# Kernel optimization log

Hardware: AMD Instinct MI355X
Metric: run time of the kernel (lower is better)

Reference implementation:

```python
import jax, jax.numpy as jnp
import numpy as np

B, N, H = 512, 100, 768
I = 2 * H  # intermediate_dim default = hidden_dim * 2
NUM_ANS = 16
MAX_ANS = 15
LN_EPS = 1e-5


def setup_inputs() -> dict:
    key = jax.random.key(0)
    ks = jax.random.split(key, 7)
    s = 0.02
    return {
        "v_emb": jax.random.normal(ks[0], (B, N, H), dtype=jnp.float32),
        "W1": jax.random.normal(ks[1], (H, I), dtype=jnp.float32) * s,
        "b1": jax.random.normal(ks[2], (I,), dtype=jnp.float32) * s,
        "gamma": jnp.ones((I,), dtype=jnp.float32),
        "beta": jnp.zeros((I,), dtype=jnp.float32),
        "W2": jax.random.normal(ks[3], (I, 1), dtype=jnp.float32) * s,
        "b2": jax.random.normal(ks[4], (1,), dtype=jnp.float32) * s,
    }


def reference(v_emb, W1, b1, gamma, beta, W2, b2):
    # Linear -> GELU (exact/erf, torch nn.GELU default) -> LayerNorm -> Linear
    h = jnp.einsum("bnh,hi->bni", v_emb, W1) + b1            # [B,N,I]
    h = jax.nn.gelu(h, approximate=False)
    mu = jnp.mean(h, axis=-1, keepdims=True)
    var = jnp.mean(jnp.square(h - mu), axis=-1, keepdims=True)
    h = (h - mu) * jax.lax.rsqrt(var + LN_EPS) * gamma + beta
    scores = jnp.einsum("bni,io->bno", h, W2) + b2           # [B,N,1]
    scores = jax.nn.sigmoid(scores)                           # sigmoid=True branch
    pred = jnp.sum(scores, axis=1)                            # [B,1]
    # pred_to_logits: vectorized round + clamp + one-hot scatter
    # str(int(round(p))) in {'0'..'15'} -> that id; negative -> 0; overflow -> max_ans
    aid = jnp.clip(jnp.round(pred[:, 0]).astype(jnp.int32), 0, MAX_ANS)
    logits = jax.nn.one_hot(aid, NUM_ANS, dtype=scores.dtype)  # [B,16]
    # original returns dict: scores, final_attention_map (==scores), pred, logits
    return scores, pred, logits
```

## Files before the change

### kernel.cpp

```cpp
#include <hip/hip_runtime.h>
#include <hip/hip_bf16.h>
#include <cstdint>
#include <cstddef>

#define BB   512
#define NN   100
#define HH   768
#define II   1536
#define MM   (BB*NN)

typedef __bf16 bf16;
typedef __bf16 bf16x4 __attribute__((ext_vector_type(4)));
typedef __bf16 bf16x8 __attribute__((ext_vector_type(8)));
typedef float  f32x4  __attribute__((ext_vector_type(4)));

__device__ __forceinline__ void gld_lds16(const bf16* g, bf16* l) {
    __builtin_amdgcn_global_load_lds(
        (const __attribute__((address_space(1))) void*)g,
        (__attribute__((address_space(3))) void*)l, 16, 0, 0);
}

__global__ __launch_bounds__(256) void prep_kernel(
    const float* __restrict__ W1, const float* __restrict__ gamma,
    const float* __restrict__ beta, const float* __restrict__ W2,
    const float* __restrict__ b2,
    bf16* __restrict__ Wp, float* __restrict__ gw, float* __restrict__ scal)
{
    int bid = blockIdx.x;
    if (bid < 1152) {
        int t  = bid * 256 + threadIdx.x;
        int n  = t % II;
        int k0 = (t / II) * 4;
        bf16x4 v;
        v[0] = (bf16)W1[(size_t)(k0+0)*II + n];
        v[1] = (bf16)W1[(size_t)(k0+1)*II + n];
        v[2] = (bf16)W1[(size_t)(k0+2)*II + n];
        v[3] = (bf16)W1[(size_t)(k0+3)*II + n];
        *(bf16x4*)&Wp[(size_t)n*HH + k0] = v;
    } else if (bid == 1152) {
        for (int j = threadIdx.x; j < II; j += 256)
            gw[j] = gamma[j] * W2[j];
    } else {
        float s1 = 0.f, s2 = 0.f;
        for (int j = threadIdx.x; j < II; j += 256) {
            float w2 = W2[j];
            s1 += gamma[j] * w2;
            s2 += beta[j]  * w2;
        }
        #pragma unroll
        for (int off = 32; off; off >>= 1) {
            s1 += __shfl_down(s1, off, 64);
            s2 += __shfl_down(s2, off, 64);
        }
        __shared__ float a1[4], a2[4];
        int lane = threadIdx.x & 63, w = threadIdx.x >> 6;
        if (lane == 0) { a1[w] = s1; a2[w] = s2; }
        __syncthreads();
        if (threadIdx.x == 0) {
            scal[0] = a1[0] + a1[1] + a1[2] + a1[3];
            scal[1] = a2[0] + a2[1] + a2[2] + a2[3] + b2[0];
        }
    }
}

__global__ __launch_bounds__(256) void conv_kernel(
    const float* __restrict__ A, bf16* __restrict__ Apk)
{
    const size_t i = ((size_t)blockIdx.x * 256 + threadIdx.x) * 4;
    float4 v = *(const float4*)&A[i];
    bf16x4 o = { (bf16)v.x, (bf16)v.y, (bf16)v.z, (bf16)v.w };
    *(bf16x4*)&Apk[i] = o;
}

template <bool PK>
__global__ __launch_bounds__(256) void gemm_part(
    const float* __restrict__ Af, const bf16* __restrict__ Apk,
    const bf16* __restrict__ Wp, const float* __restrict__ b1,
    const float* __restrict__ gw, float* __restrict__ part)
{
    __shared__ bf16  As[128 * 64];
    __shared__ bf16  Bs[128 * 64];
    __shared__ float sred[2][128][3];

    const int tid  = threadIdx.x;
    const int nb   = blockIdx.x % 12;
    const int mb   = blockIdx.x / 12;
    const int lane = tid & 63;
    const int w    = tid >> 6;
    const int wm   = w >> 1;
    const int wn   = w & 1;
    const int m15  = lane & 15;
    const int q    = lane >> 4;
    const int row0 = mb * 128;

    const int rsub = tid >> 3;
    const int kgA  = (tid & 7) ^ (rsub & 7);
    const size_t gbase = (size_t)rsub * HH + (size_t)kgA * 8;
    const int    lbase = tid * 8;

    const bf16* Bg = Wp + (size_t)(nb * 128) * HH;

    f32x4 acc[4][4] = {};

    for (int kt = 0; kt < 12; ++kt) {
        const int koff = kt * 64;
        if (PK) {
            const bf16* Ag = Apk + (size_t)row0 * HH;
            #pragma unroll
            for (int it = 0; it < 4; ++it) {
                size_t go = gbase + (size_t)it * 32 * HH + koff;
                int    lo = lbase + it * 2048;
                gld_lds16(Ag + go, &As[lo]);
                gld_lds16(Bg + go, &Bs[lo]);
            }
        } else {
            #pragma unroll
            for (int it = 0; it < 4; ++it) {
                size_t go = gbase + (size_t)it * 32 * HH + koff;
                gld_lds16(Bg + go, &Bs[lbase + it * 2048]);
            }
            #pragma unroll
            for (int it = 0; it < 4; ++it) {
                const float* src = Af + (size_t)(row0 + it*32 + rsub) * HH
                                      + koff + kgA * 8;
                float4 v0 = *(const float4*)(src);
                float4 v1 = *(const float4*)(src + 4);
                bf16x8 o = { (bf16)v0.x, (bf16)v0.y, (bf16)v0.z, (bf16)v0.w,
                             (bf16)v1.x, (bf16)v1.y, (bf16)v1.z, (bf16)v1.w };
                *(bf16x8*)&As[lbase + it * 2048] = o;
            }
        }
        asm volatile("s_waitcnt vmcnt(0)" ::: "memory");
        __syncthreads();

        #pragma unroll
        for (int kb = 0; kb < 2; ++kb) {
            const int swz = (((kb * 4 + q) ^ (m15 & 7)) * 8);
            bf16x8 af[4], bfr[4];
            #pragma unroll
            for (int mt = 0; mt < 4; ++mt)
                af[mt] = *(const bf16x8*)&As[(wm*64 + mt*16 + m15) * 64 + swz];
            #pragma unroll
            for (int nt = 0; nt < 4; ++nt)
                bfr[nt] = *(const bf16x8*)&Bs[(wn*64 + nt*16 + m15) * 64 + swz];
            #pragma unroll
            for (int mt = 0; mt < 4; ++mt)
                #pragma unroll
                for (int nt = 0; nt < 4; ++nt)
                    acc[mt][nt] = __builtin_amdgcn_mfma_f32_16x16x32_bf16(
                        af[mt], bfr[nt], acc[mt][nt], 0, 0, 0);
        }
        __syncthreads();
    }

    float bv[4], gv[4];
    #pragma unroll
    for (int nt = 0; nt < 4; ++nt) {
        const int col = nb*128 + wn*64 + nt*16 + m15;
        bv[nt] = b1[col];
        gv[nt] = gw[col];
    }

    #pragma unroll
    for (int mt = 0; mt < 4; ++mt) {
        #pragma unroll
        for (int r = 0; r < 4; ++r) {
            float x0 = 0.f, x1 = 0.f, x2 = 0.f;
            #pragma unroll
            for (int nt = 0; nt < 4; ++nt) {
                float x = acc[mt][nt][r] + bv[nt];
                float g = 0.5f * x * (1.0f + erff(x * 0.70710678118654752f));
                x0 += g; x1 += g * g; x2 += g * gv[nt];
            }
            #pragma unroll
            for (int off = 8; off; off >>= 1) {
                x0 += __shfl_down(x0, off, 16);
                x1 += __shfl_down(x1, off, 16);
                x2 += __shfl_down(x2, off, 16);
            }
            if (m15 == 0) {
                const int rl = wm*64 + mt*16 + q*4 + r;
                sred[wn][rl][0] = x0;
                sred[wn][rl][1] = x1;
                sred[wn][rl][2] = x2;
            }
        }
    }
    __syncthreads();

    if (tid < 128) {
        const size_t rg = (size_t)(row0 + tid);
        #pragma unroll
        for (int s = 0; s < 3; ++s)
            part[rg * 36 + s * 12 + nb] = sred[0][tid][s] + sred[1][tid][s];
    }
}

__global__ __launch_bounds__(256) void ln_finish(
    const float* __restrict__ part, const float* __restrict__ scal,
    float* __restrict__ scores)
{
    const size_t row = (size_t)blockIdx.x * 256 + threadIdx.x;
    const float* p = part + row * 36;
    float Sh = 0.f, Shh = 0.f, Shg = 0.f;
    #pragma unroll
    for (int j = 0; j < 12; ++j) {
        Sh  += p[j];
        Shh += p[12 + j];
        Shg += p[24 + j];
    }
    const float mu   = Sh * (1.0f / II);
    const float var  = Shh * (1.0f / II) - mu * mu;
    const float rstd = rsqrtf(var + 1e-5f);
    const float z    = rstd * (Shg - mu * scal[0]) + scal[1];
    scores[row] = 1.0f / (1.0f + __expf(-z));
}

__global__ __launch_bounds__(128) void pred_logits(
    const float* __restrict__ scores, float* __restrict__ out_pred,
    float* __restrict__ out_logits)
{
    const int b = blockIdx.x, t = threadIdx.x;
    float v = (t < NN) ? scores[b * NN + t] : 0.0f;
    #pragma unroll
    for (int off = 32; off; off >>= 1) v += __shfl_down(v, off, 64);
    __shared__ float ssum[2];
    const int lane = t & 63, w = t >> 6;
    if (lane == 0) ssum[w] = v;
    __syncthreads();
    const float p = ssum[0] + ssum[1];
    if (t == 0) out_pred[b] = p;
    if (t < 16) {
        int aid = (int)rintf(p);
        aid = aid < 0 ? 0 : (aid > 15 ? 15 : aid);
        out_logits[b * 16 + t] = (t == aid) ? 1.0f : 0.0f;
    }
}

extern "C" void kernel_launch(void* const* d_in, const int* in_sizes, int n_in,
                              void* d_out, int out_size, void* d_ws, size_t ws_size,
                              hipStream_t stream)
{
    const float* v_emb = (const float*)d_in[0];
    const float* W1    = (const float*)d_in[1];
    const float* b1    = (const float*)d_in[2];
    const float* gamma = (const float*)d_in[3];
    const float* beta  = (const float*)d_in[4];
    const float* W2    = (const float*)d_in[5];
    const float* b2    = (const float*)d_in[6];

    char* ws = (char*)d_ws;
    size_t off = 0;
    bf16*  Wp   = (bf16*)(ws + off);  off += (size_t)II * HH * 2;
    float* gw   = (float*)(ws + off); off += (size_t)II * 4;
    float* scal = (float*)(ws + off); off += 256;
    float* part = (float*)(ws + off); off += (size_t)MM * 36 * 4;
    bf16*  Apk  = (bf16*)(ws + off);
    const size_t need_pk = off + (size_t)MM * HH * 2;
    const bool   use_pk  = (ws_size >= need_pk);

    float* out       = (float*)d_out;
    float* o_scores  = out;
    float* o_pred    = out + MM;
    float* o_logits  = out + MM + BB;

    hipLaunchKernelGGL(prep_kernel, dim3(1154), dim3(256), 0, stream,
                       W1, gamma, beta, W2, b2, Wp, gw, scal);
    if (use_pk) {
        hipLaunchKernelGGL(conv_kernel, dim3((MM * HH) / (256 * 4)), dim3(256),
                           0, stream, v_emb, Apk);
        hipLaunchKernelGGL((gemm_part<true>), dim3((MM / 128) * 12), dim3(256),
                           0, stream, v_emb, Apk, Wp, b1, gw, part);
    } else {
        hipLaunchKernelGGL((gemm_part<false>), dim3((MM / 128) * 12), dim3(256),
                           0, stream, v_emb, Apk, Wp, b1, gw, part);
    }
    hipLaunchKernelGGL(ln_finish, dim3(MM / 256), dim3(256), 0, stream,
                       part, scal, o_scores);
    hipLaunchKernelGGL(pred_logits, dim3(BB), dim3(128), 0, stream,
                       o_scores, o_pred, o_logits);
}
```

Before: 455.3 us.

## Use polynomial GELU, remap blocks by XCD, fuse LN finish with pred

Replaces erff in the GEMM epilogue with an Abramowitz-Stegun polynomial erf built on a hardware reciprocal and exp. Remaps block indices so consecutive blocks land on the same XCD, aiming for better L2 reuse of A and W tiles. Transposes the partial-sum layout so it is coalesced and merges the layernorm finish kernel into the per-batch pred/logits kernel, saving one launch and one scores round trip. The non-packed fallback path is removed, so the workspace is now assumed large enough, and the approximate erf adds some error.

```diff
diff --git a/kernel.cpp b/kernel.cpp
--- a/kernel.cpp
+++ b/kernel.cpp
@@ -18,6 +18,20 @@
     __builtin_amdgcn_global_load_lds(
         (const __attribute__((address_space(1))) void*)g,
         (__attribute__((address_space(3))) void*)l, 16, 0, 0);
+}
+
+__device__ __forceinline__ float fast_gelu(float x) {
+    const float ax = fabsf(x) * 0.70710678118654752f;
+    const float t  = __builtin_amdgcn_rcpf(fmaf(0.3275911f, ax, 1.0f));
+    float p = fmaf(1.061405429f, t, -1.453152027f);
+    p = fmaf(p, t, 1.421413741f);
+    p = fmaf(p, t, -0.284496736f);
+    p = fmaf(p, t, 0.254829592f);
+    p = p * t;
+    const float e    = __expf(-ax * ax);
+    const float erfa = fmaf(-p, e, 1.0f);
+    const float erfx = copysignf(erfa, x);
+    return 0.5f * x * (1.0f + erfx);
 }
 
 __global__ __launch_bounds__(256) void prep_kernel(
@@ -72,19 +86,19 @@
     *(bf16x4*)&Apk[i] = o;
 }
 
-template <bool PK>
 __global__ __launch_bounds__(256) void gemm_part(
-    const float* __restrict__ Af, const bf16* __restrict__ Apk,
-    const bf16* __restrict__ Wp, const float* __restrict__ b1,
-    const float* __restrict__ gw, float* __restrict__ part)
+    const bf16* __restrict__ Apk, const bf16* __restrict__ Wp,
+    const float* __restrict__ b1, const float* __restrict__ gw,
+    float* __restrict__ part)
 {
     __shared__ bf16  As[128 * 64];
     __shared__ bf16  Bs[128 * 64];
     __shared__ float sred[2][128][3];
 
     const int tid  = threadIdx.x;
-    const int nb   = blockIdx.x % 12;
-    const int mb   = blockIdx.x / 12;
+    const int lin  = (blockIdx.x % 8) * 600 + blockIdx.x / 8;
+    const int mb   = lin / 12;
+    const int nb   = lin % 12;
     const int lane = tid & 63;
     const int w    = tid >> 6;
     const int wm   = w >> 1;
@@ -98,37 +112,19 @@
     const size_t gbase = (size_t)rsub * HH + (size_t)kgA * 8;
     const int    lbase = tid * 8;
 
-    const bf16* Bg = Wp + (size_t)(nb * 128) * HH;
+    const bf16* Ag = Apk + (size_t)row0 * HH;
+    const bf16* Bg = Wp  + (size_t)(nb * 128) * HH;
 
     f32x4 acc[4][4] = {};
 
     for (int kt = 0; kt < 12; ++kt) {
         const int koff = kt * 64;
-        if (PK) {
-            const bf16* Ag = Apk + (size_t)row0 * HH;
-            #pragma unroll
-            for (int it = 0; it < 4; ++it) {
-                size_t go = gbase + (size_t)it * 32 * HH + koff;
-                int    lo = lbase + it * 2048;
-                gld_lds16(Ag + go, &As[lo]);
-                gld_lds16(Bg + go, &Bs[lo]);
-            }
-        } else {
-            #pragma unroll
-            for (int it = 0; it < 4; ++it) {
-                size_t go = gbase + (size_t)it * 32 * HH + koff;
-                gld_lds16(Bg + go, &Bs[lbase + it * 2048]);
-            }
-            #pragma unroll
-            for (int it = 0; it < 4; ++it) {
-                const float* src = Af + (size_t)(row0 + it*32 + rsub) * HH
-                                      + koff + kgA * 8;
-                float4 v0 = *(const float4*)(src);
-                float4 v1 = *(const float4*)(src + 4);
-                bf16x8 o = { (bf16)v0.x, (bf16)v0.y, (bf16)v0.z, (bf16)v0.w,
-                             (bf16)v1.x, (bf16)v1.y, (bf16)v1.z, (bf16)v1.w };
-                *(bf16x8*)&As[lbase + it * 2048] = o;
-            }
+        #pragma unroll
+        for (int it = 0; it < 4; ++it) {
+            size_t go = gbase + (size_t)it * 32 * HH + koff;
+            int    lo = lbase + it * 2048;
+            gld_lds16(Ag + go, &As[lo]);
+            gld_lds16(Bg + go, &Bs[lo]);
         }
         asm volatile("s_waitcnt vmcnt(0)" ::: "memory");
         __syncthreads();
@@ -168,8 +164,7 @@
             float x0 = 0.f, x1 = 0.f, x2 = 0.f;
             #pragma unroll
             for (int nt = 0; nt < 4; ++nt) {
-                float x = acc[mt][nt][r] + bv[nt];
-                float g = 0.5f * x * (1.0f + erff(x * 0.70710678118654752f));
+                float g = fast_gelu(acc[mt][nt][r] + bv[nt]);
                 x0 += g; x1 += g * g; x2 += g * gv[nt];
             }
             #pragma unroll
@@ -189,39 +184,38 @@
     __syncthreads();
 
     if (tid < 128) {
-        const size_t rg = (size_t)(row0 + tid);
+        const size_t rg = (size_t)row0 + tid;
         #pragma unroll
         for (int s = 0; s < 3; ++s)
-            part[rg * 36 + s * 12 + nb] = sred[0][tid][s] + sred[1][tid][s];
-    }
-}
-
-__global__ __launch_bounds__(256) void ln_finish(
+            part[(size_t)s * 12 * MM + (size_t)nb * MM + rg]
+                = sred[0][tid][s] + sred[1][tid][s];
+    }
+}
+
+__global__ __launch_bounds__(128) void score_pred(
     const float* __restrict__ part, const float* __restrict__ scal,
-    float* __restrict__ scores)
-{
-    const size_t row = (size_t)blockIdx.x * 256 + threadIdx.x;
-    const float* p = part + row * 36;
-    float Sh = 0.f, Shh = 0.f, Shg = 0.f;
-    #pragma unroll
-    for (int j = 0; j < 12; ++j) {
-        Sh  += p[j];
-        Shh += p[12 + j];
-        Shg += p[24 + j];
-    }
-    const float mu   = Sh * (1.0f / II);
-    const float var  = Shh * (1.0f / II) - mu * mu;
-    const float rstd = rsqrtf(var + 1e-5f);
-    const float z    = rstd * (Shg - mu * scal[0]) + scal[1];
-    scores[row] = 1.0f / (1.0f + __expf(-z));
-}
-
-__global__ __launch_bounds__(128) void pred_logits(
-    const float* __restrict__ scores, float* __restrict__ out_pred,
-    float* __restrict__ out_logits)
+    float* __restrict__ o_scores, float* __restrict__ o_pred,
+    float* __restrict__ o_logits)
 {
     const int b = blockIdx.x, t = threadIdx.x;
-    float v = (t < NN) ? scores[b * NN + t] : 0.0f;
+    float s = 0.f;
+    if (t < NN) {
+        const size_t row = (size_t)b * NN + t;
+        float Sh = 0.f, Shh = 0.f, Shg = 0.f;
+        #pragma unroll
+        for (int j = 0; j < 12; ++j) {
+            Sh  += part[(size_t)0*12*MM + (size_t)j*MM + row];
+            Shh += part[(size_t)1*12*MM + (size_t)j*MM + row];
+            Shg += part[(size_t)2*12*MM + (size_t)j*MM + row];
+        }
+        const float mu   = Sh * (1.0f / II);
+        const float var  = Shh * (1.0f / II) - mu * mu;
+        const float rstd = rsqrtf(var + 1e-5f);
+        const float z    = rstd * (Shg - mu * scal[0]) + scal[1];
+        s = 1.0f / (1.0f + __expf(-z));
+        o_scores[row] = s;
+    }
+    float v = s;
     #pragma unroll
     for (int off = 32; off; off >>= 1) v += __shfl_down(v, off, 64);
     __shared__ float ssum[2];
@@ -229,11 +223,11 @@
     if (lane == 0) ssum[w] = v;
     __syncthreads();
     const float p = ssum[0] + ssum[1];
-    if (t == 0) out_pred[b] = p;
+    if (t == 0) o_pred[b] = p;
     if (t < 16) {
         int aid = (int)rintf(p);
         aid = aid < 0 ? 0 : (aid > 15 ? 15 : aid);
-        out_logits[b * 16 + t] = (t == aid) ? 1.0f : 0.0f;
+        o_logits[b * 16 + t] = (t == aid) ? 1.0f : 0.0f;
     }
 }
 
@@ -256,8 +250,6 @@
     float* scal = (float*)(ws + off); off += 256;
     float* part = (float*)(ws + off); off += (size_t)MM * 36 * 4;
     bf16*  Apk  = (bf16*)(ws + off);
-    const size_t need_pk = off + (size_t)MM * HH * 2;
-    const bool   use_pk  = (ws_size >= need_pk);
 
     float* out       = (float*)d_out;
     float* o_scores  = out;
@@ -266,17 +258,10 @@
 
     hipLaunchKernelGGL(prep_kernel, dim3(1154), dim3(256), 0, stream,
                        W1, gamma, beta, W2, b2, Wp, gw, scal);
-    if (use_pk) {
-        hipLaunchKernelGGL(conv_kernel, dim3((MM * HH) / (256 * 4)), dim3(256),
-                           0, stream, v_emb, Apk);
-        hipLaunchKernelGGL((gemm_part<true>), dim3((MM / 128) * 12), dim3(256),
-                           0, stream, v_emb, Apk, Wp, b1, gw, part);
-    } else {
-        hipLaunchKernelGGL((gemm_part<false>), dim3((MM / 128) * 12), dim3(256),
-                           0, stream, v_emb, Apk, Wp, b1, gw, part);
-    }
-    hipLaunchKernelGGL(ln_finish, dim3(MM / 256), dim3(256), 0, stream,
-                       part, scal, o_scores);
-    hipLaunchKernelGGL(pred_logits, dim3(BB), dim3(128), 0, stream,
-                       o_scores, o_pred, o_logits);
-}
+    hipLaunchKernelGGL(conv_kernel, dim3((MM * HH) / (256 * 4)), dim3(256),
+                       0, stream, v_emb, Apk);
+    hipLaunchKernelGGL(gemm_part, dim3((MM / 128) * 12), dim3(256),
+                       0, stream, Apk, Wp, b1, gw, part);
+    hipLaunchKernelGGL(score_pred, dim3(BB), dim3(128), 0, stream,
+                       part, scal, o_scores, o_pred, o_logits);
+}
```

Measured after the change: 429.0 us. 1.06x faster.
